# Performance work log

Measured on AMD Instinct MI355X. Metric: run time of the kernel, lower is better.

## Reference

```python
import jax, jax.numpy as jnp
import numpy as np

B, N, D, H = 2, 2048, 128, 128  # batch, n_nodes, node_dim, hidden_dim
HQ = H // 4
EPS_DIST = 1e-8
EPS_LN = 1e-5


def setup_inputs() -> dict:
    key = jax.random.key(0)
    ks = jax.random.split(key, 12)
    s = 0.02
    return {
        "h": jax.random.normal(ks[0], (B, N, D), jnp.float32),
        "coords": jax.random.uniform(ks[1], (B, N, 2), jnp.float32),
        "Wq": jax.random.normal(ks[2], (D, H), jnp.float32) * s,
        "bq": jnp.zeros((H,), jnp.float32),
        "Wk": jax.random.normal(ks[3], (D, H), jnp.float32) * s,
        "bk": jnp.zeros((H,), jnp.float32),
        "Wv": jax.random.normal(ks[4], (D, H), jnp.float32) * s,
        "bv": jnp.zeros((H,), jnp.float32),
        "Wd1": jax.random.normal(ks[5], (1, HQ), jnp.float32) * s,
        "bd1": jnp.zeros((HQ,), jnp.float32),
        "Wd2": jax.random.normal(ks[6], (HQ, 1), jnp.float32) * s,
        "bd2": jnp.zeros((1,), jnp.float32),
        "Wo": jax.random.normal(ks[7], (H, D), jnp.float32) * s,
        "bo": jnp.zeros((D,), jnp.float32),
        "gamma": jnp.ones((D,), jnp.float32),
        "beta": jnp.zeros((D,), jnp.float32),
    }


def reference(h, coords, Wq, bq, Wk, bk, Wv, bv, Wd1, bd1, Wd2, bd2, Wo, bo, gamma, beta):
    q = h @ Wq + bq                      # (B, N, H)
    k = h @ Wk + bk
    v = h @ Wv + bv
    scores = jnp.einsum('bnh,bmh->bnm', q, k) / jnp.sqrt(jnp.float32(H))  # (B,N,N)
    # pairwise Euclidean distances
    diff = coords[:, :, None, :] - coords[:, None, :, :]                  # (B,N,N,2)
    dist = jnp.sqrt(jnp.sum(diff * diff, axis=-1, keepdims=True) + EPS_DIST)  # (B,N,N,1)
    hmid = jax.nn.silu(dist @ Wd1 + bd1)                                  # (B,N,N,HQ)
    dist_bias = (hmid @ Wd2 + bd2)[..., 0]                                # (B,N,N)
    attn = jax.nn.softmax(scores + dist_bias, axis=-1)
    out = jnp.einsum('bnm,bmh->bnh', attn, v)                             # (B,N,H)
    out = jax.nn.silu(out @ Wo + bo)                                      # (B,N,D)
    res = h + out
    mu = jnp.mean(res, axis=-1, keepdims=True)
    var = jnp.mean((res - mu) ** 2, axis=-1, keepdims=True)
    return (res - mu) / jnp.sqrt(var + EPS_LN) * gamma + beta
```

## Files before the change

kernel.cpp:

```cpp
#include <hip/hip_runtime.h>
#include <hip/hip_bf16.h>

#define B_ 2
#define N_ 2048
#define D_ 128
#define H_ 128
#define ROWS_ (B_*N_)
#define KS_ 16
#define DMAX_ 1.4143f
#define SCALE_ 0.08838834764831845f
#define LOG2E_ 1.4426950408889634f

typedef __bf16 bf16x8 __attribute__((ext_vector_type(8)));
typedef float  f32x4  __attribute__((ext_vector_type(4)));
typedef unsigned short ushort8 __attribute__((ext_vector_type(8)));

#if __has_builtin(__builtin_amdgcn_exp2f)
#define EXP2F_ __builtin_amdgcn_exp2f
#else
#define EXP2F_ exp2f
#endif
#if __has_builtin(__builtin_amdgcn_sqrtf)
#define SQRTF_ __builtin_amdgcn_sqrtf
#else
#define SQRTF_ sqrtf
#endif

#define Q_OFF    0
#define K_OFF    (ROWS_*H_*2)
#define V_OFF    (2*ROWS_*H_*2)
#define CF_OFF   (3*ROWS_*H_*2)
#define L_OFF    (CF_OFF + 64)
#define OP_OFF   (L_OFF + ROWS_*32*4)

__global__ __launch_bounds__(256) void qkv_mfma(
    const float* __restrict__ h,
    const float* __restrict__ Wq, const float* __restrict__ bq,
    const float* __restrict__ Wk, const float* __restrict__ bk,
    const float* __restrict__ Wv, const float* __restrict__ bv,
    const float* __restrict__ Wd1, const float* __restrict__ bd1,
    const float* __restrict__ Wd2, const float* __restrict__ bd2,
    __bf16* __restrict__ qb, __bf16* __restrict__ kb, __bf16* __restrict__ vb,
    float* __restrict__ cf)
{
    __shared__ __align__(16) __bf16 Wl[32][144];
    const int t = threadIdx.x;
    const int y = blockIdx.y;
    const int which = y >> 2, c0 = (y & 3) * 32;
    const float* W    = which == 0 ? Wq : (which == 1 ? Wk : Wv);
    const float* bias = which == 0 ? bq : (which == 1 ? bk : bv);
    __bf16* outp      = which == 0 ? qb : (which == 1 ? kb : vb);
    const float scale = which == 0 ? (SCALE_ * LOG2E_) : 1.f;

    if (blockIdx.x == 0 && y == 0 && t < 64) {
        const int j = t & 31;
        const float w1 = Wd1[j], b1 = bd1[j];
        const float w2h = Wd2[j] * 0.5f;
        float gv[3];
        #pragma unroll
        for (int i = 0; i < 3; ++i) {
            float d = (DMAX_ * 0.5f) * (float)i;
            float x = fmaf(d, w1, b1);
            gv[i] = (x / (1.f + __expf(-x))) * w2h;
        }
        #pragma unroll
        for (int i = 0; i < 3; ++i)
            #pragma unroll
            for (int off = 1; off < 64; off <<= 1) gv[i] += __shfl_xor(gv[i], off);
        if (t == 0) {
            const float bd2v = bd2[0];
            float g0 = (gv[0] + bd2v) * LOG2E_, g1 = (gv[1] + bd2v) * LOG2E_,
                  g2 = (gv[2] + bd2v) * LOG2E_;
            cf[0] = g0;
            cf[1] = -1.5f * g0 + 2.f * g1 - 0.5f * g2;
            cf[2] =  0.5f * g0 - g1 + 0.5f * g2;
        }
    }

    #pragma unroll
    for (int i = 0; i < 16; ++i) {
        int idx = t + i * 256, k = idx >> 5, cc = idx & 31;
        Wl[cc][k] = (__bf16)W[k * 128 + c0 + cc];
    }
    __syncthreads();

    const int wid = t >> 6, lane = t & 63, l16 = lane & 15, g = lane >> 4;
    const int row0 = blockIdx.x * 64 + wid * 16;

    bf16x8 af[4];
    const float* arow = h + (size_t)(row0 + l16) * 128;
    #pragma unroll
    for (int kk = 0; kk < 4; ++kk) {
        float4 a0 = *(const float4*)(arow + kk * 32 + g * 8);
        float4 a1 = *(const float4*)(arow + kk * 32 + g * 8 + 4);
        af[kk] = (bf16x8){ (__bf16)a0.x, (__bf16)a0.y, (__bf16)a0.z, (__bf16)a0.w,
                           (__bf16)a1.x, (__bf16)a1.y, (__bf16)a1.z, (__bf16)a1.w };
    }

    f32x4 acc0 = {0.f,0.f,0.f,0.f}, acc1 = {0.f,0.f,0.f,0.f};
    #pragma unroll
    for (int kk = 0; kk < 4; ++kk) {
        bf16x8 f0 = *(const bf16x8*)&Wl[l16][kk * 32 + g * 8];
        acc0 = __builtin_amdgcn_mfma_f32_16x16x32_bf16(af[kk], f0, acc0, 0, 0, 0);
    }
    #pragma unroll
    for (int kk = 0; kk < 4; ++kk) {
        bf16x8 f1 = *(const bf16x8*)&Wl[16 + l16][kk * 32 + g * 8];
        acc1 = __builtin_amdgcn_mfma_f32_16x16x32_bf16(af[kk], f1, acc1, 0, 0, 0);
    }
    const float bv0 = bias[c0 + l16], bv1 = bias[c0 + 16 + l16];
    #pragma unroll
    for (int i = 0; i < 4; ++i) {
        size_t r = (size_t)(row0 + g * 4 + i) * 128;
        outp[r + c0 + l16]      = (__bf16)((acc0[i] + bv0) * scale);
        outp[r + c0 + 16 + l16] = (__bf16)((acc1[i] + bv1) * scale);
    }
}

template<int KSP>
__global__ __launch_bounds__(256, 3) void attn_kernel(
    const __bf16* __restrict__ qb, const __bf16* __restrict__ kb, const __bf16* __restrict__ vb,
    const float* __restrict__ coords, const float* __restrict__ cfp,
    unsigned int* __restrict__ Opb32, float* __restrict__ Larr)
{
    constexpr int KPP = N_ / KSP;
    constexpr int NT  = KPP / 32;
    constexpr float CSC = 2.0f / DMAX_;

    __shared__ __align__(16) unsigned int Vsu[2][128][20];
    __shared__ __align__(16) __bf16 Pl[4][2][16][40];

    const int t    = threadIdx.x;
    const int wid  = t >> 6;
    const int lane = t & 63;
    const int l16  = lane & 15;
    const int g    = lane >> 4;
    const int qb0  = blockIdx.x * 128 + wid * 16;
    const int p    = blockIdx.y;
    const int b    = blockIdx.x >> 4;

    const float c0 = cfp[0], c1 = cfp[1], c2 = cfp[2];

    bf16x8 qf[2][4];
    #pragma unroll
    for (int tt = 0; tt < 2; ++tt) {
        const __bf16* qrow = qb + (size_t)(qb0 + tt * 64 + l16) * H_;
        #pragma unroll
        for (int kk = 0; kk < 4; ++kk) qf[tt][kk] = *(const bf16x8*)(qrow + kk * 32 + g * 8);
    }

    float cx[2][4], cy[2][4];
    #pragma unroll
    for (int tt = 0; tt < 2; ++tt)
        #pragma unroll
        for (int i = 0; i < 4; ++i) {
            int qr = qb0 + tt * 64 + g * 4 + i;
            cx[tt][i] = coords[qr * 2] * CSC; cy[tt][i] = coords[qr * 2 + 1] * CSC;
        }

    float l_i[2][4] = {{0.f,0.f,0.f,0.f},{0.f,0.f,0.f,0.f}};
    f32x4 O0[8], O1[8];
    #pragma unroll
    for (int c = 0; c < 8; ++c) { O0[c] = (f32x4){0.f,0.f,0.f,0.f}; O1[c] = (f32x4){0.f,0.f,0.f,0.f}; }

    const int kp = t & 15, co = t >> 4;
    const int kgbase = (b << 11) + p * KPP;

    {
        const __bf16* sp = vb + (size_t)(kgbase + 2 * kp) * H_ + co * 8;
        bf16x8 va = *(const bf16x8*)sp;
        bf16x8 vb2 = *(const bf16x8*)(sp + H_);
        ushort8 ua = __builtin_bit_cast(ushort8, va);
        ushort8 ub = __builtin_bit_cast(ushort8, vb2);
        #pragma unroll
        for (int j = 0; j < 8; ++j)
            Vsu[0][co * 8 + j][kp] = (unsigned)ua[j] | ((unsigned)ub[j] << 16);
    }

    for (int kt = 0; kt < NT; ++kt) {
        __syncthreads();

        bf16x8 nva, nvb;
        if (kt + 1 < NT) {
            const __bf16* sp = vb + (size_t)(kgbase + (kt + 1) * 32 + 2 * kp) * H_ + co * 8;
            nva = *(const bf16x8*)sp;
            nvb = *(const bf16x8*)(sp + H_);
        }

        const int kg = kgbase + kt * 32;
        #pragma unroll
        for (int mt = 0; mt < 2; ++mt) {
            bf16x8 kf[4];
            const __bf16* krow = kb + (size_t)(kg + mt * 16 + l16) * H_;
            #pragma unroll
            for (int kk = 0; kk < 4; ++kk) kf[kk] = *(const bf16x8*)(krow + kk * 32 + g * 8);

            f32x4 acc0 = {0.f,0.f,0.f,0.f}, acc1 = {0.f,0.f,0.f,0.f};
            #pragma unroll
            for (int kk = 0; kk < 4; ++kk)
                acc0 = __builtin_amdgcn_mfma_f32_16x16x32_bf16(qf[0][kk], kf[kk], acc0, 0, 0, 0);
            #pragma unroll
            for (int kk = 0; kk < 4; ++kk)
                acc1 = __builtin_amdgcn_mfma_f32_16x16x32_bf16(qf[1][kk], kf[kk], acc1, 0, 0, 0);

            float2 kc = *(const float2*)&coords[(kg + mt * 16 + l16) * 2];
            const float kx = kc.x * CSC, ky = kc.y * CSC;
            #pragma unroll
            for (int i = 0; i < 4; ++i) {
                float dx = cx[0][i] - kx, dy = cy[0][i] - ky;
                float s = SQRTF_(fmaf(dx, dx, fmaf(dy, dy, 2e-8f)));
                float pe = EXP2F_(acc0[i] + fmaf(fmaf(c2, s, c1), s, c0));
                l_i[0][i] += pe;
                Pl[wid][0][g * 4 + i][mt * 16 + l16] = (__bf16)pe;
            }
            #pragma unroll
            for (int i = 0; i < 4; ++i) {
                float dx = cx[1][i] - kx, dy = cy[1][i] - ky;
                float s = SQRTF_(fmaf(dx, dx, fmaf(dy, dy, 2e-8f)));
                float pe = EXP2F_(acc1[i] + fmaf(fmaf(c2, s, c1), s, c0));
                l_i[1][i] += pe;
                Pl[wid][1][g * 4 + i][mt * 16 + l16] = (__bf16)pe;
            }
        }

        if (kt + 1 < NT) {
            ushort8 ua = __builtin_bit_cast(ushort8, nva);
            ushort8 ub = __builtin_bit_cast(ushort8, nvb);
            #pragma unroll
            for (int j = 0; j < 8; ++j)
                Vsu[(kt + 1) & 1][co * 8 + j][kp] = (unsigned)ua[j] | ((unsigned)ub[j] << 16);
        }

        bf16x8 pf0 = *(const bf16x8*)&Pl[wid][0][l16][g * 8];
        bf16x8 pf1 = *(const bf16x8*)&Pl[wid][1][l16][g * 8];
        #pragma unroll
        for (int c = 0; c < 8; ++c) {
            bf16x8 vf = *(const bf16x8*)&Vsu[kt & 1][c * 16 + l16][g * 4];
            O0[c] = __builtin_amdgcn_mfma_f32_16x16x32_bf16(pf0, vf, O0[c], 0, 0, 0);
            O1[c] = __builtin_amdgcn_mfma_f32_16x16x32_bf16(pf1, vf, O1[c], 0, 0, 0);
        }
    }

    #pragma unroll
    for (int tt = 0; tt < 2; ++tt) {
        const size_t rpbase = (size_t)p * (ROWS_ / 2) + ((qb0 + tt * 64) >> 1) + g * 2;
        #pragma unroll
        for (int c = 0; c < 8; ++c)
            #pragma unroll
            for (int ip = 0; ip < 2; ++ip) {
                float lo_f = tt ? O1[c][2 * ip]     : O0[c][2 * ip];
                float hi_f = tt ? O1[c][2 * ip + 1] : O0[c][2 * ip + 1];
                unsigned lo = __builtin_bit_cast(unsigned, lo_f);
                unsigned hi = __builtin_bit_cast(unsigned, hi_f);
                Opb32[(rpbase + ip) * H_ + c * 16 + l16] = (hi & 0xffff0000u) | (lo >> 16);
            }
    }
    #pragma unroll
    for (int tt = 0; tt < 2; ++tt)
        #pragma unroll
        for (int i = 0; i < 4; ++i) {
            float lv = l_i[tt][i];
            lv += __shfl_xor(lv, 1); lv += __shfl_xor(lv, 2);
            lv += __shfl_xor(lv, 4); lv += __shfl_xor(lv, 8);
            if (l16 == 0) Larr[(qb0 + tt * 64 + g * 4 + i) * KSP + p] = lv;
        }
}

template<int KSP>
__global__ __launch_bounds__(256) void final_kernel(
    const unsigned int* __restrict__ Opb32, const float* __restrict__ Larr,
    const float* __restrict__ h, const float* __restrict__ Wo, const float* __restrict__ bo,
    const float* __restrict__ gamma, const float* __restrict__ beta, float* __restrict__ out)
{
    __shared__ __align__(16) float as_[8][128];
    __shared__ float redS[4][4], redQ[4][4];
    const int t = threadIdx.x;
    const int c = t & 127;
    const int rh = t >> 7;
    const int bx = blockIdx.x;
    const int row0 = (bx & 31) * 128 + (bx >> 5) * 8;

    #pragma unroll
    for (int pr = 0; pr < 2; ++pr) {
        int r0 = rh * 4 + pr * 2;
        int row = row0 + r0;
        size_t rp = (size_t)row >> 1;
        float accL = 0.f, accH = 0.f, lsumL = 0.f, lsumH = 0.f;
        #pragma unroll
        for (int p = 0; p < KSP; ++p) {
            unsigned v = Opb32[((size_t)p * (ROWS_ / 2) + rp) * H_ + c];
            accL += __uint_as_float(v << 16);
            accH += __uint_as_float(v & 0xffff0000u);
        }
        #pragma unroll
        for (int q4 = 0; q4 < KSP / 4; ++q4) {
            f32x4 lL = *(const f32x4*)&Larr[row * KSP + q4 * 4];
            f32x4 lH = *(const f32x4*)&Larr[(row + 1) * KSP + q4 * 4];
            lsumL += lL[0] + lL[1] + lL[2] + lL[3];
            lsumH += lH[0] + lH[1] + lH[2] + lH[3];
        }
        as_[r0][c]     = accL / lsumL;
        as_[r0 + 1][c] = accH / lsumH;
    }
    __syncthreads();

    float acc4[4] = {0.f, 0.f, 0.f, 0.f};
    #pragma unroll 4
    for (int d4 = 0; d4 < 32; ++d4) {
        float w0 = Wo[(d4 * 4 + 0) * 128 + c];
        float w1 = Wo[(d4 * 4 + 1) * 128 + c];
        float w2 = Wo[(d4 * 4 + 2) * 128 + c];
        float w3 = Wo[(d4 * 4 + 3) * 128 + c];
        #pragma unroll
        for (int r = 0; r < 4; ++r) {
            f32x4 a_ = *(const f32x4*)&as_[rh * 4 + r][d4 * 4];
            acc4[r] = fmaf(a_[0], w0, acc4[r]);
            acc4[r] = fmaf(a_[1], w1, acc4[r]);
            acc4[r] = fmaf(a_[2], w2, acc4[r]);
            acc4[r] = fmaf(a_[3], w3, acc4[r]);
        }
    }

    const float bov = bo[c], gv = gamma[c], bvv = beta[c];
    const int wv = t >> 6;
    float res[4];
    #pragma unroll
    for (int r = 0; r < 4; ++r) {
        float x = acc4[r] + bov;
        float sl = x / (1.f + __expf(-x));
        res[r] = h[(size_t)(row0 + rh * 4 + r) * 128 + c] + sl;
    }

    #pragma unroll
    for (int r = 0; r < 4; ++r) {
        float s1 = res[r], s2 = res[r] * res[r];
        #pragma unroll
        for (int off = 32; off >= 1; off >>= 1) {
            s1 += __shfl_xor(s1, off);
            s2 += __shfl_xor(s2, off);
        }
        if ((t & 63) == 0) { redS[wv][r] = s1; redQ[wv][r] = s2; }
    }
    __syncthreads();
    #pragma unroll
    for (int r = 0; r < 4; ++r) {
        float sum = redS[2 * rh][r] + redS[2 * rh + 1][r];
        float sq  = redQ[2 * rh][r] + redQ[2 * rh + 1][r];
        float mu  = sum * (1.f / 128.f);
        float var = sq * (1.f / 128.f) - mu * mu;
        out[(size_t)(row0 + rh * 4 + r) * 128 + c] = (res[r] - mu) * rsqrtf(var + 1e-5f) * gv + bvv;
    }
}

extern "C" void kernel_launch(void* const* d_in, const int* in_sizes, int n_in,
                              void* d_out, int out_size, void* d_ws, size_t ws_size,
                              hipStream_t stream)
{
    const float* h      = (const float*)d_in[0];
    const float* coords = (const float*)d_in[1];
    const float* Wq = (const float*)d_in[2];  const float* bq = (const float*)d_in[3];
    const float* Wk = (const float*)d_in[4];  const float* bk = (const float*)d_in[5];
    const float* Wv = (const float*)d_in[6];  const float* bv = (const float*)d_in[7];
    const float* Wd1 = (const float*)d_in[8]; const float* bd1 = (const float*)d_in[9];
    const float* Wd2 = (const float*)d_in[10];const float* bd2 = (const float*)d_in[11];
    const float* Wo = (const float*)d_in[12]; const float* bo = (const float*)d_in[13];
    const float* gamma = (const float*)d_in[14]; const float* beta = (const float*)d_in[15];

    char* ws = (char*)d_ws;
    __bf16* qb = (__bf16*)(ws + Q_OFF);
    __bf16* kb = (__bf16*)(ws + K_OFF);
    __bf16* vb = (__bf16*)(ws + V_OFF);
    float* cf           = (float*)(ws + CF_OFF);
    float* Larr         = (float*)(ws + L_OFF);
    unsigned int* Opb32 = (unsigned int*)(ws + OP_OFF);

    qkv_mfma<<<dim3(64, 12), 256, 0, stream>>>(h, Wq, bq, Wk, bk, Wv, bv,
                                               Wd1, bd1, Wd2, bd2, qb, kb, vb, cf);
    attn_kernel<KS_><<<dim3(32, KS_), 256, 0, stream>>>(qb, kb, vb, coords, cf, Opb32, Larr);
    final_kernel<KS_><<<ROWS_ / 8, 256, 0, stream>>>(Opb32, Larr, h, Wo, bo, gamma, beta, (float*)d_out);
}
```

Measured before the change: 48.27 us.

## Fuse QKV, attention and output stages into one cooperative kernel with grid syncs

Replaces the three separate launches (QKV projection, split-K attention, output projection plus LayerNorm) with one cooperative kernel of 512 blocks that uses grid.sync between the phases, removing launch gaps and inter-kernel drains. The QKV phase is re-tiled to 384 blocks and the attention phase processes two 64-row query tiles per block. If the cooperative launch fails, it falls back to the three kernels with the split count raised to 32. Grid-wide barriers add their own synchronisation cost and cap occupancy at 512 resident blocks, and the bid-range work split leaves some blocks idle in the first phase.

```diff
diff --git a/kernel.cpp b/kernel.cpp
--- a/kernel.cpp
+++ b/kernel.cpp
@@ -1,12 +1,15 @@
 #include <hip/hip_runtime.h>
 #include <hip/hip_bf16.h>
+#include <hip/hip_cooperative_groups.h>
+
+namespace cg = cooperative_groups;
 
 #define B_ 2
 #define N_ 2048
 #define D_ 128
 #define H_ 128
 #define ROWS_ (B_*N_)
-#define KS_ 16
+#define KSC_ 16
 #define DMAX_ 1.4143f
 #define SCALE_ 0.08838834764831845f
 #define LOG2E_ 1.4426950408889634f
@@ -32,6 +35,7 @@
 #define CF_OFF   (3*ROWS_*H_*2)
 #define L_OFF    (CF_OFF + 64)
 #define OP_OFF   (L_OFF + ROWS_*32*4)
+
 
 __global__ __launch_bounds__(256) void qkv_mfma(
     const float* __restrict__ h,
@@ -352,6 +356,319 @@
     }
 }
 
+__global__ __launch_bounds__(256, 3) void fused_kernel(
+    const float* __restrict__ h, const float* __restrict__ coords,
+    const float* __restrict__ Wq, const float* __restrict__ bq,
+    const float* __restrict__ Wk, const float* __restrict__ bk,
+    const float* __restrict__ Wv, const float* __restrict__ bv,
+    const float* __restrict__ Wd1, const float* __restrict__ bd1,
+    const float* __restrict__ Wd2, const float* __restrict__ bd2,
+    const float* __restrict__ Wo, const float* __restrict__ bo,
+    const float* __restrict__ gamma, const float* __restrict__ beta,
+    __bf16* qb, __bf16* kb, __bf16* vb,
+    float* cf, unsigned int* Opb32, float* Larr, float* out)
+{
+    __shared__ __align__(16) char smem[30720];
+
+    cg::grid_group grid = cg::this_grid();
+    const int bid  = blockIdx.x;
+    const int t    = threadIdx.x;
+    const int wid  = t >> 6;
+    const int lane = t & 63;
+    const int l16  = lane & 15;
+    const int g    = lane >> 4;
+
+    if (bid < 384) {
+        const int rb = bid / 6, sub = bid - rb * 6;
+        const int m = sub >> 1, ch = sub & 1;
+        const float* W    = m == 0 ? Wq : (m == 1 ? Wk : Wv);
+        const float* bias = m == 0 ? bq : (m == 1 ? bk : bv);
+        __bf16* outp      = m == 0 ? qb : (m == 1 ? kb : vb);
+        const float scale = m == 0 ? (SCALE_ * LOG2E_) : 1.f;
+        const int c0 = ch * 64;
+
+        __bf16 (*Wl)[136] = reinterpret_cast<__bf16 (*)[136]>(smem);
+        #pragma unroll
+        for (int i = 0; i < 32; ++i) {
+            int idx = t + i * 256, k = idx >> 6, cc = idx & 63;
+            Wl[cc][k] = (__bf16)W[k * 128 + c0 + cc];
+        }
+        __syncthreads();
+
+        const int row0 = rb * 64 + wid * 16;
+        bf16x8 af[4];
+        const float* arow = h + (size_t)(row0 + l16) * 128;
+        #pragma unroll
+        for (int kk = 0; kk < 4; ++kk) {
+            float4 a0 = *(const float4*)(arow + kk * 32 + g * 8);
+            float4 a1 = *(const float4*)(arow + kk * 32 + g * 8 + 4);
+            af[kk] = (bf16x8){ (__bf16)a0.x, (__bf16)a0.y, (__bf16)a0.z, (__bf16)a0.w,
+                               (__bf16)a1.x, (__bf16)a1.y, (__bf16)a1.z, (__bf16)a1.w };
+        }
+        #pragma unroll
+        for (int ct = 0; ct < 4; ++ct) {
+            f32x4 acc = {0.f, 0.f, 0.f, 0.f};
+            #pragma unroll
+            for (int kk = 0; kk < 4; ++kk) {
+                bf16x8 bf = *(const bf16x8*)&Wl[ct * 16 + l16][kk * 32 + g * 8];
+                acc = __builtin_amdgcn_mfma_f32_16x16x32_bf16(af[kk], bf, acc, 0, 0, 0);
+            }
+            const float bvv = bias[c0 + ct * 16 + l16];
+            #pragma unroll
+            for (int i = 0; i < 4; ++i)
+                outp[(size_t)(row0 + g * 4 + i) * 128 + c0 + ct * 16 + l16] =
+                    (__bf16)((acc[i] + bvv) * scale);
+        }
+    } else if (bid == 384 && t < 64) {
+        const int j = t & 31;
+        const float w1 = Wd1[j], b1 = bd1[j];
+        const float w2h = Wd2[j] * 0.5f;
+        float gv[3];
+        #pragma unroll
+        for (int i = 0; i < 3; ++i) {
+            float d = (DMAX_ * 0.5f) * (float)i;
+            float x = fmaf(d, w1, b1);
+            gv[i] = (x / (1.f + __expf(-x))) * w2h;
+        }
+        #pragma unroll
+        for (int i = 0; i < 3; ++i)
+            #pragma unroll
+            for (int off = 1; off < 64; off <<= 1) gv[i] += __shfl_xor(gv[i], off);
+        if (t == 0) {
+            const float bd2v = bd2[0];
+            float g0 = (gv[0] + bd2v) * LOG2E_, g1 = (gv[1] + bd2v) * LOG2E_,
+                  g2 = (gv[2] + bd2v) * LOG2E_;
+            cf[0] = g0;
+            cf[1] = -1.5f * g0 + 2.f * g1 - 0.5f * g2;
+            cf[2] =  0.5f * g0 - g1 + 0.5f * g2;
+        }
+    }
+
+    grid.sync();
+
+    {
+        constexpr int KPP = N_ / KSC_;
+        constexpr int NT  = KPP / 32;
+        constexpr float CSC = 2.0f / DMAX_;
+        unsigned int (*Vsu)[128][20] = reinterpret_cast<unsigned int (*)[128][20]>(smem);
+        __bf16 (*Pl)[2][16][40]      = reinterpret_cast<__bf16 (*)[2][16][40]>(smem + 20480);
+
+        const int p  = bid & 15;
+        const int xq = bid >> 4;
+        const int qb0 = xq * 128 + wid * 16;
+        const int b   = xq >> 4;
+
+        const float c0 = cf[0], c1 = cf[1], c2 = cf[2];
+
+        bf16x8 qf[2][4];
+        #pragma unroll
+        for (int tt = 0; tt < 2; ++tt) {
+            const __bf16* qrow = qb + (size_t)(qb0 + tt * 64 + l16) * H_;
+            #pragma unroll
+            for (int kk = 0; kk < 4; ++kk) qf[tt][kk] = *(const bf16x8*)(qrow + kk * 32 + g * 8);
+        }
+
+        float cx[2][4], cy[2][4];
+        #pragma unroll
+        for (int tt = 0; tt < 2; ++tt)
+            #pragma unroll
+            for (int i = 0; i < 4; ++i) {
+                int qr = qb0 + tt * 64 + g * 4 + i;
+                cx[tt][i] = coords[qr * 2] * CSC; cy[tt][i] = coords[qr * 2 + 1] * CSC;
+            }
+
+        float l_i[2][4] = {{0.f,0.f,0.f,0.f},{0.f,0.f,0.f,0.f}};
+        f32x4 O0[8], O1[8];
+        #pragma unroll
+        for (int c = 0; c < 8; ++c) { O0[c] = (f32x4){0.f,0.f,0.f,0.f}; O1[c] = (f32x4){0.f,0.f,0.f,0.f}; }
+
+        const int kp = t & 15, co = t >> 4;
+        const int kgbase = (b << 11) + p * KPP;
+
+        __syncthreads();
+        {
+            const __bf16* sp = vb + (size_t)(kgbase + 2 * kp) * H_ + co * 8;
+            bf16x8 va = *(const bf16x8*)sp;
+            bf16x8 vb2 = *(const bf16x8*)(sp + H_);
+            ushort8 ua = __builtin_bit_cast(ushort8, va);
+            ushort8 ub = __builtin_bit_cast(ushort8, vb2);
+            #pragma unroll
+            for (int j = 0; j < 8; ++j)
+                Vsu[0][co * 8 + j][kp] = (unsigned)ua[j] | ((unsigned)ub[j] << 16);
+        }
+
+        for (int kt = 0; kt < NT; ++kt) {
+            __syncthreads();
+
+            bf16x8 nva, nvb;
+            if (kt + 1 < NT) {
+                const __bf16* sp = vb + (size_t)(kgbase + (kt + 1) * 32 + 2 * kp) * H_ + co * 8;
+                nva = *(const bf16x8*)sp;
+                nvb = *(const bf16x8*)(sp + H_);
+            }
+
+            const int kg = kgbase + kt * 32;
+            #pragma unroll
+            for (int mt = 0; mt < 2; ++mt) {
+                bf16x8 kf[4];
+                const __bf16* krow = kb + (size_t)(kg + mt * 16 + l16) * H_;
+                #pragma unroll
+                for (int kk = 0; kk < 4; ++kk) kf[kk] = *(const bf16x8*)(krow + kk * 32 + g * 8);
+
+                f32x4 acc0 = {0.f,0.f,0.f,0.f}, acc1 = {0.f,0.f,0.f,0.f};
+                #pragma unroll
+                for (int kk = 0; kk < 4; ++kk)
+                    acc0 = __builtin_amdgcn_mfma_f32_16x16x32_bf16(qf[0][kk], kf[kk], acc0, 0, 0, 0);
+                #pragma unroll
+                for (int kk = 0; kk < 4; ++kk)
+                    acc1 = __builtin_amdgcn_mfma_f32_16x16x32_bf16(qf[1][kk], kf[kk], acc1, 0, 0, 0);
+
+                float2 kc = *(const float2*)&coords[(kg + mt * 16 + l16) * 2];
+                const float kx = kc.x * CSC, ky = kc.y * CSC;
+                #pragma unroll
+                for (int i = 0; i < 4; ++i) {
+                    float dx = cx[0][i] - kx, dy = cy[0][i] - ky;
+                    float s = SQRTF_(fmaf(dx, dx, fmaf(dy, dy, 2e-8f)));
+                    float pe = EXP2F_(acc0[i] + fmaf(fmaf(c2, s, c1), s, c0));
+                    l_i[0][i] += pe;
+                    Pl[wid][0][g * 4 + i][mt * 16 + l16] = (__bf16)pe;
+                }
+                #pragma unroll
+                for (int i = 0; i < 4; ++i) {
+                    float dx = cx[1][i] - kx, dy = cy[1][i] - ky;
+                    float s = SQRTF_(fmaf(dx, dx, fmaf(dy, dy, 2e-8f)));
+                    float pe = EXP2F_(acc1[i] + fmaf(fmaf(c2, s, c1), s, c0));
+                    l_i[1][i] += pe;
+                    Pl[wid][1][g * 4 + i][mt * 16 + l16] = (__bf16)pe;
+                }
+            }
+
+            if (kt + 1 < NT) {
+                ushort8 ua = __builtin_bit_cast(ushort8, nva);
+                ushort8 ub = __builtin_bit_cast(ushort8, nvb);
+                #pragma unroll
+                for (int j = 0; j < 8; ++j)
+                    Vsu[(kt + 1) & 1][co * 8 + j][kp] = (unsigned)ua[j] | ((unsigned)ub[j] << 16);
+            }
+
+            bf16x8 pf0 = *(const bf16x8*)&Pl[wid][0][l16][g * 8];
+            bf16x8 pf1 = *(const bf16x8*)&Pl[wid][1][l16][g * 8];
+            #pragma unroll
+            for (int c = 0; c < 8; ++c) {
+                bf16x8 vf = *(const bf16x8*)&Vsu[kt & 1][c * 16 + l16][g * 4];
+                O0[c] = __builtin_amdgcn_mfma_f32_16x16x32_bf16(pf0, vf, O0[c], 0, 0, 0);
+                O1[c] = __builtin_amdgcn_mfma_f32_16x16x32_bf16(pf1, vf, O1[c], 0, 0, 0);
+            }
+        }
+
+        #pragma unroll
+        for (int tt = 0; tt < 2; ++tt) {
+            const size_t rpbase = (size_t)p * (ROWS_ / 2) + ((qb0 + tt * 64) >> 1) + g * 2;
+            #pragma unroll
+            for (int c = 0; c < 8; ++c)
+                #pragma unroll
+                for (int ip = 0; ip < 2; ++ip) {
+                    float lo_f = tt ? O1[c][2 * ip]     : O0[c][2 * ip];
+                    float hi_f = tt ? O1[c][2 * ip + 1] : O0[c][2 * ip + 1];
+                    unsigned lo = __builtin_bit_cast(unsigned, lo_f);
+                    unsigned hi = __builtin_bit_cast(unsigned, hi_f);
+                    Opb32[(rpbase + ip) * H_ + c * 16 + l16] = (hi & 0xffff0000u) | (lo >> 16);
+                }
+        }
+        #pragma unroll
+        for (int tt = 0; tt < 2; ++tt)
+            #pragma unroll
+            for (int i = 0; i < 4; ++i) {
+                float lv = l_i[tt][i];
+                lv += __shfl_xor(lv, 1); lv += __shfl_xor(lv, 2);
+                lv += __shfl_xor(lv, 4); lv += __shfl_xor(lv, 8);
+                if (l16 == 0) Larr[(qb0 + tt * 64 + g * 4 + i) * KSC_ + p] = lv;
+            }
+    }
+
+    grid.sync();
+
+    {
+        float (*as_)[128] = reinterpret_cast<float (*)[128]>(smem);
+        float (*redS)[4]  = reinterpret_cast<float (*)[4]>(smem + 4096);
+        float (*redQ)[4]  = reinterpret_cast<float (*)[4]>(smem + 4096 + 64);
+        const int c  = t & 127;
+        const int rh = t >> 7;
+        const int row0 = bid * 8;
+
+        #pragma unroll
+        for (int pr = 0; pr < 2; ++pr) {
+            int r0 = rh * 4 + pr * 2;
+            int row = row0 + r0;
+            size_t rp = (size_t)row >> 1;
+            float accL = 0.f, accH = 0.f, lsumL = 0.f, lsumH = 0.f;
+            #pragma unroll
+            for (int p = 0; p < KSC_; ++p) {
+                unsigned v = Opb32[((size_t)p * (ROWS_ / 2) + rp) * H_ + c];
+                accL += __uint_as_float(v << 16);
+                accH += __uint_as_float(v & 0xffff0000u);
+            }
+            #pragma unroll
+            for (int q4 = 0; q4 < KSC_ / 4; ++q4) {
+                f32x4 lL = *(const f32x4*)&Larr[row * KSC_ + q4 * 4];
+                f32x4 lH = *(const f32x4*)&Larr[(row + 1) * KSC_ + q4 * 4];
+                lsumL += lL[0] + lL[1] + lL[2] + lL[3];
+                lsumH += lH[0] + lH[1] + lH[2] + lH[3];
+            }
+            as_[r0][c]     = accL / lsumL;
+            as_[r0 + 1][c] = accH / lsumH;
+        }
+        __syncthreads();
+
+        float acc4[4] = {0.f, 0.f, 0.f, 0.f};
+        #pragma unroll 4
+        for (int d4 = 0; d4 < 32; ++d4) {
+            float w0 = Wo[(d4 * 4 + 0) * 128 + c];
+            float w1 = Wo[(d4 * 4 + 1) * 128 + c];
+            float w2 = Wo[(d4 * 4 + 2) * 128 + c];
+            float w3 = Wo[(d4 * 4 + 3) * 128 + c];
+            #pragma unroll
+            for (int r = 0; r < 4; ++r) {
+                f32x4 a_ = *(const f32x4*)&as_[rh * 4 + r][d4 * 4];
+                acc4[r] = fmaf(a_[0], w0, acc4[r]);
+                acc4[r] = fmaf(a_[1], w1, acc4[r]);
+                acc4[r] = fmaf(a_[2], w2, acc4[r]);
+                acc4[r] = fmaf(a_[3], w3, acc4[r]);
+            }
+        }
+
+        const float bov = bo[c], gv = gamma[c], bvv = beta[c];
+        const int wv = t >> 6;
+        float res[4];
+        #pragma unroll
+        for (int r = 0; r < 4; ++r) {
+            float x = acc4[r] + bov;
+            float sl = x / (1.f + __expf(-x));
+            res[r] = h[(size_t)(row0 + rh * 4 + r) * 128 + c] + sl;
+        }
+
+        #pragma unroll
+        for (int r = 0; r < 4; ++r) {
+            float s1 = res[r], s2 = res[r] * res[r];
+            #pragma unroll
+            for (int off = 32; off >= 1; off >>= 1) {
+                s1 += __shfl_xor(s1, off);
+                s2 += __shfl_xor(s2, off);
+            }
+            if ((t & 63) == 0) { redS[wv][r] = s1; redQ[wv][r] = s2; }
+        }
+        __syncthreads();
+        #pragma unroll
+        for (int r = 0; r < 4; ++r) {
+            float sum = redS[2 * rh][r] + redS[2 * rh + 1][r];
+            float sq  = redQ[2 * rh][r] + redQ[2 * rh + 1][r];
+            float mu  = sum * (1.f / 128.f);
+            float var = sq * (1.f / 128.f) - mu * mu;
+            out[(size_t)(row0 + rh * 4 + r) * 128 + c] = (res[r] - mu) * rsqrtf(var + 1e-5f) * gv + bvv;
+        }
+    }
+}
+
 extern "C" void kernel_launch(void* const* d_in, const int* in_sizes, int n_in,
                               void* d_out, int out_size, void* d_ws, size_t ws_size,
                               hipStream_t stream)
@@ -373,9 +690,23 @@
     float* cf           = (float*)(ws + CF_OFF);
     float* Larr         = (float*)(ws + L_OFF);
     unsigned int* Opb32 = (unsigned int*)(ws + OP_OFF);
-
-    qkv_mfma<<<dim3(64, 12), 256, 0, stream>>>(h, Wq, bq, Wk, bk, Wv, bv,
-                                               Wd1, bd1, Wd2, bd2, qb, kb, vb, cf);
-    attn_kernel<KS_><<<dim3(32, KS_), 256, 0, stream>>>(qb, kb, vb, coords, cf, Opb32, Larr);
-    final_kernel<KS_><<<ROWS_ / 8, 256, 0, stream>>>(Opb32, Larr, h, Wo, bo, gamma, beta, (float*)d_out);
+    float* out          = (float*)d_out;
+
+    void* args[] = {
+        (void*)&h, (void*)&coords,
+        (void*)&Wq, (void*)&bq, (void*)&Wk, (void*)&bk, (void*)&Wv, (void*)&bv,
+        (void*)&Wd1, (void*)&bd1, (void*)&Wd2, (void*)&bd2,
+        (void*)&Wo, (void*)&bo, (void*)&gamma, (void*)&beta,
+        (void*)&qb, (void*)&kb, (void*)&vb,
+        (void*)&cf, (void*)&Opb32, (void*)&Larr, (void*)&out
+    };
+    hipError_t err = hipLaunchCooperativeKernel((const void*)fused_kernel,
+                                                dim3(512), dim3(256), args, 0, stream);
+    if (err != hipSuccess) {
+        (void)hipGetLastError();
+        qkv_mfma<<<dim3(64, 12), 256, 0, stream>>>(h, Wq, bq, Wk, bk, Wv, bv,
+                                                   Wd1, bd1, Wd2, bd2, qb, kb, vb, cf);
+        attn_kernel<32><<<dim3(32, 32), 256, 0, stream>>>(qb, kb, vb, coords, cf, Opb32, Larr);
+        final_kernel<32><<<ROWS_ / 8, 256, 0, stream>>>(Opb32, Larr, h, Wo, bo, gamma, beta, out);
+    }
 }
```

Result: slower. 180.5 us (+274.0%).

## Split attention work across eight waves with one query tile each

Applied to the files above, without the earlier changes.

The attention kernel now launches 512 threads per block, and each wave processes a single 16-row query tile instead of two. This halves per-wave accumulator and fragment registers, allowing more resident waves to hide exp/sqrt and memory latency. In exchange, each K fragment and V LDS read is amortized over half as many MFMAs, so K loads from cache and LDS traffic double. Only the first 256 threads stage V into shared memory.

```diff
diff --git a/kernel.cpp b/kernel.cpp
--- a/kernel.cpp
+++ b/kernel.cpp
@@ -118,7 +118,7 @@
 }
 
 template<int KSP>
-__global__ __launch_bounds__(256, 3) void attn_kernel(
+__global__ __launch_bounds__(512, 2) void attn_kernel(
     const __bf16* __restrict__ qb, const __bf16* __restrict__ kb, const __bf16* __restrict__ vb,
     const float* __restrict__ coords, const float* __restrict__ cfp,
     unsigned int* __restrict__ Opb32, float* __restrict__ Larr)
@@ -128,7 +128,7 @@
     constexpr float CSC = 2.0f / DMAX_;
 
     __shared__ __align__(16) unsigned int Vsu[2][128][20];
-    __shared__ __align__(16) __bf16 Pl[4][2][16][40];
+    __shared__ __align__(16) __bf16 Pl[8][16][40];
 
     const int t    = threadIdx.x;
     const int wid  = t >> 6;
@@ -141,32 +141,27 @@
 
     const float c0 = cfp[0], c1 = cfp[1], c2 = cfp[2];
 
-    bf16x8 qf[2][4];
-    #pragma unroll
-    for (int tt = 0; tt < 2; ++tt) {
-        const __bf16* qrow = qb + (size_t)(qb0 + tt * 64 + l16) * H_;
-        #pragma unroll
-        for (int kk = 0; kk < 4; ++kk) qf[tt][kk] = *(const bf16x8*)(qrow + kk * 32 + g * 8);
-    }
-
-    float cx[2][4], cy[2][4];
-    #pragma unroll
-    for (int tt = 0; tt < 2; ++tt)
-        #pragma unroll
-        for (int i = 0; i < 4; ++i) {
-            int qr = qb0 + tt * 64 + g * 4 + i;
-            cx[tt][i] = coords[qr * 2] * CSC; cy[tt][i] = coords[qr * 2 + 1] * CSC;
-        }
-
-    float l_i[2][4] = {{0.f,0.f,0.f,0.f},{0.f,0.f,0.f,0.f}};
-    f32x4 O0[8], O1[8];
-    #pragma unroll
-    for (int c = 0; c < 8; ++c) { O0[c] = (f32x4){0.f,0.f,0.f,0.f}; O1[c] = (f32x4){0.f,0.f,0.f,0.f}; }
+    bf16x8 qf[4];
+    const __bf16* qrow = qb + (size_t)(qb0 + l16) * H_;
+    #pragma unroll
+    for (int kk = 0; kk < 4; ++kk) qf[kk] = *(const bf16x8*)(qrow + kk * 32 + g * 8);
+
+    float cx[4], cy[4];
+    #pragma unroll
+    for (int i = 0; i < 4; ++i) {
+        int qr = qb0 + g * 4 + i;
+        cx[i] = coords[qr * 2] * CSC; cy[i] = coords[qr * 2 + 1] * CSC;
+    }
+
+    float l_i[4] = {0.f, 0.f, 0.f, 0.f};
+    f32x4 O[8];
+    #pragma unroll
+    for (int c = 0; c < 8; ++c) O[c] = (f32x4){0.f, 0.f, 0.f, 0.f};
 
     const int kp = t & 15, co = t >> 4;
     const int kgbase = (b << 11) + p * KPP;
 
-    {
+    if (t < 256) {
         const __bf16* sp = vb + (size_t)(kgbase + 2 * kp) * H_ + co * 8;
         bf16x8 va = *(const bf16x8*)sp;
         bf16x8 vb2 = *(const bf16x8*)(sp + H_);
@@ -181,7 +176,7 @@
         __syncthreads();
 
         bf16x8 nva, nvb;
-        if (kt + 1 < NT) {
+        if (t < 256 && kt + 1 < NT) {
             const __bf16* sp = vb + (size_t)(kgbase + (kt + 1) * 32 + 2 * kp) * H_ + co * 8;
             nva = *(const bf16x8*)sp;
             nvb = *(const bf16x8*)(sp + H_);
@@ -195,35 +190,24 @@
             #pragma unroll
             for (int kk = 0; kk < 4; ++kk) kf[kk] = *(const bf16x8*)(krow + kk * 32 + g * 8);
 
-            f32x4 acc0 = {0.f,0.f,0.f,0.f}, acc1 = {0.f,0.f,0.f,0.f};
+            f32x4 acc = {0.f, 0.f, 0.f, 0.f};
             #pragma unroll
             for (int kk = 0; kk < 4; ++kk)
-                acc0 = __builtin_amdgcn_mfma_f32_16x16x32_bf16(qf[0][kk], kf[kk], acc0, 0, 0, 0);
-            #pragma unroll
-            for (int kk = 0; kk < 4; ++kk)
-                acc1 = __builtin_amdgcn_mfma_f32_16x16x32_bf16(qf[1][kk], kf[kk], acc1, 0, 0, 0);
+                acc = __builtin_amdgcn_mfma_f32_16x16x32_bf16(qf[kk], kf[kk], acc, 0, 0, 0);
 
             float2 kc = *(const float2*)&coords[(kg + mt * 16 + l16) * 2];
             const float kx = kc.x * CSC, ky = kc.y * CSC;
             #pragma unroll
             for (int i = 0; i < 4; ++i) {
-                float dx = cx[0][i] - kx, dy = cy[0][i] - ky;
+                float dx = cx[i] - kx, dy = cy[i] - ky;
                 float s = SQRTF_(fmaf(dx, dx, fmaf(dy, dy, 2e-8f)));
-                float pe = EXP2F_(acc0[i] + fmaf(fmaf(c2, s, c1), s, c0));
-                l_i[0][i] += pe;
-                Pl[wid][0][g * 4 + i][mt * 16 + l16] = (__bf16)pe;
+                float pe = EXP2F_(acc[i] + fmaf(fmaf(c2, s, c1), s, c0));
+                l_i[i] += pe;
+                Pl[wid][g * 4 + i][mt * 16 + l16] = (__bf16)pe;
             }
-            #pragma unroll
-            for (int i = 0; i < 4; ++i) {
-                float dx = cx[1][i] - kx, dy = cy[1][i] - ky;
-                float s = SQRTF_(fmaf(dx, dx, fmaf(dy, dy, 2e-8f)));
-                float pe = EXP2F_(acc1[i] + fmaf(fmaf(c2, s, c1), s, c0));
-                l_i[1][i] += pe;
-                Pl[wid][1][g * 4 + i][mt * 16 + l16] = (__bf16)pe;
-            }
-        }
-
-        if (kt + 1 < NT) {
+        }
+
+        if (t < 256 && kt + 1 < NT) {
             ushort8 ua = __builtin_bit_cast(ushort8, nva);
             ushort8 ub = __builtin_bit_cast(ushort8, nvb);
             #pragma unroll
@@ -231,39 +215,32 @@
                 Vsu[(kt + 1) & 1][co * 8 + j][kp] = (unsigned)ua[j] | ((unsigned)ub[j] << 16);
         }
 
-        bf16x8 pf0 = *(const bf16x8*)&Pl[wid][0][l16][g * 8];
-        bf16x8 pf1 = *(const bf16x8*)&Pl[wid][1][l16][g * 8];
+        bf16x8 pf = *(const bf16x8*)&Pl[wid][l16][g * 8];
         #pragma unroll
         for (int c = 0; c < 8; ++c) {
             bf16x8 vf = *(const bf16x8*)&Vsu[kt & 1][c * 16 + l16][g * 4];
-            O0[c] = __builtin_amdgcn_mfma_f32_16x16x32_bf16(pf0, vf, O0[c], 0, 0, 0);
-            O1[c] = __builtin_amdgcn_mfma_f32_16x16x32_bf16(pf1, vf, O1[c], 0, 0, 0);
-        }
-    }
-
-    #pragma unroll
-    for (int tt = 0; tt < 2; ++tt) {
-        const size_t rpbase = (size_t)p * (ROWS_ / 2) + ((qb0 + tt * 64) >> 1) + g * 2;
+            O[c] = __builtin_amdgcn_mfma_f32_16x16x32_bf16(pf, vf, O[c], 0, 0, 0);
+        }
+    }
+
+    {
+        const size_t rpbase = (size_t)p * (ROWS_ / 2) + (qb0 >> 1) + g * 2;
         #pragma unroll
         for (int c = 0; c < 8; ++c)
             #pragma unroll
             for (int ip = 0; ip < 2; ++ip) {
-                float lo_f = tt ? O1[c][2 * ip]     : O0[c][2 * ip];
-                float hi_f = tt ? O1[c][2 * ip + 1] : O0[c][2 * ip + 1];
-                unsigned lo = __builtin_bit_cast(unsigned, lo_f);
-                unsigned hi = __builtin_bit_cast(unsigned, hi_f);
+                unsigned lo = __builtin_bit_cast(unsigned, O[c][2 * ip]);
+                unsigned hi = __builtin_bit_cast(unsigned, O[c][2 * ip + 1]);
                 Opb32[(rpbase + ip) * H_ + c * 16 + l16] = (hi & 0xffff0000u) | (lo >> 16);
             }
     }
     #pragma unroll
-    for (int tt = 0; tt < 2; ++tt)
-        #pragma unroll
-        for (int i = 0; i < 4; ++i) {
-            float lv = l_i[tt][i];
-            lv += __shfl_xor(lv, 1); lv += __shfl_xor(lv, 2);
-            lv += __shfl_xor(lv, 4); lv += __shfl_xor(lv, 8);
-            if (l16 == 0) Larr[(qb0 + tt * 64 + g * 4 + i) * KSP + p] = lv;
-        }
+    for (int i = 0; i < 4; ++i) {
+        float lv = l_i[i];
+        lv += __shfl_xor(lv, 1); lv += __shfl_xor(lv, 2);
+        lv += __shfl_xor(lv, 4); lv += __shfl_xor(lv, 8);
+        if (l16 == 0) Larr[(qb0 + g * 4 + i) * KSP + p] = lv;
+    }
 }
 
 template<int KSP>
@@ -376,6 +353,6 @@
 
     qkv_mfma<<<dim3(64, 12), 256, 0, stream>>>(h, Wq, bq, Wk, bk, Wv, bv,
                                                Wd1, bd1, Wd2, bd2, qb, kb, vb, cf);
-    attn_kernel<KS_><<<dim3(32, KS_), 256, 0, stream>>>(qb, kb, vb, coords, cf, Opb32, Larr);
+    attn_kernel<KS_><<<dim3(32, KS_), 512, 0, stream>>>(qb, kb, vb, coords, cf, Opb32, Larr);
     final_kernel<KS_><<<ROWS_ / 8, 256, 0, stream>>>(Opb32, Larr, h, Wo, bo, gamma, beta, (float*)d_out);
 }
```

After: 47.62 us. Within noise of the previous version (-1.4%).
